# Kernel tuning notes

Hardware: AMD Instinct MI355X
Metric: run time of the kernel (lower is better)

The kernel has to match this reference:

```python
import jax, jax.numpy as jnp
import numpy as np

N_NODES = 51200
N_EDGES = 614400
ORIG = 92
AFL = 64      # atom_fea_len
NFL = 64      # nbr_fea_len
BINS = 100
N_CONV = 3
EPS = 1e-5


def _bn(h, g, b):
    # BatchNorm1d in training mode: biased batch statistics over dim 0
    mu = h.mean(0)
    var = h.var(0)
    return (h - mu) * jax.lax.rsqrt(var + EPS) * g + b


def setup_inputs() -> dict:
    key = jax.random.key(0)
    ks = jax.random.split(key, 16)
    inp = {
        "x": jax.random.normal(ks[0], (N_NODES, ORIG), dtype=jnp.float32),
        "edge_index": jax.random.randint(ks[1], (2, N_EDGES), 0, N_NODES, dtype=jnp.int32),
        "edge_attr": jax.random.uniform(ks[2], (N_EDGES, 1), dtype=jnp.float32),
        "batchsize": 128,
        # encoder-level params
        "attention": jnp.ones((ORIG,), jnp.float32),
        "emb_W": jax.random.normal(ks[3], (ORIG, AFL), jnp.float32) / np.sqrt(ORIG),
        "emb_b": jnp.zeros((AFL,), jnp.float32),
        # per-conv params stacked along axis 0 (n_conv layers)
        "ad_w1": jax.random.normal(ks[4], (N_CONV, 1, BINS), jnp.float32),
        "ad_b1": jnp.zeros((N_CONV, BINS), jnp.float32),
        "ad_w2": jax.random.normal(ks[5], (N_CONV, BINS, BINS), jnp.float32) / np.sqrt(BINS),
        "ad_b2": jnp.zeros((N_CONV, BINS), jnp.float32),
        "ad_alpha": jax.random.uniform(ks[6], (N_CONV, 1), dtype=jnp.float32),
        "ad_lut": jax.random.uniform(ks[7], (N_CONV, BINS, NFL), dtype=jnp.float32),
        "fc_W": jax.random.normal(ks[8], (N_CONV, 2 * AFL + NFL, 2 * AFL), jnp.float32) / np.sqrt(2 * AFL + NFL),
        "fc_b": jnp.zeros((N_CONV, 2 * AFL), jnp.float32),
        "bn1_g": jnp.ones((N_CONV, 2 * AFL), jnp.float32),
        "bn1_b": jnp.zeros((N_CONV, 2 * AFL), jnp.float32),
        "bn2_g": jnp.ones((N_CONV, AFL), jnp.float32),
        "bn2_b": jnp.zeros((N_CONV, AFL), jnp.float32),
        # pre_pooling linear
        "pp_W": jax.random.normal(ks[9], (AFL, AFL), jnp.float32) / np.sqrt(AFL),
        "pp_b": jnp.zeros((AFL,), jnp.float32),
    }
    return inp


def _cgconv(h, src, dst, edge_attr, w1, b1, w2, b2, alpha, lut, fcW, fcb, g1, be1, g2, be2):
    # AutoDiscretization of the scalar edge feature -> [E, NFL]
    v2 = jax.nn.leaky_relu(edge_attr @ w1 + b1)               # [E, BINS]
    v3 = v2 @ w2 + b2 + alpha * v2                            # [E, BINS]
    e = jax.nn.softmax(v3, axis=-1) @ lut                     # [E, NFL]
    # message: gather endpoints, fused gated MLP (x_i = target, x_j = source)
    z = jnp.concatenate([h[dst], h[src], e], axis=1) @ fcW + fcb  # [E, 2*AFL]
    z = _bn(z, g1, be1)
    nbr_filter, nbr_core = jnp.split(z, 2, axis=1)
    msg = jax.nn.relu(nbr_filter) * jax.nn.relu(nbr_core)     # [E, AFL]
    # aggregate (scatter-add to target nodes) + update
    aggr = jax.ops.segment_sum(msg, dst, num_segments=N_NODES)
    return jax.nn.relu(h + _bn(aggr, g2, be2))


def reference(x, edge_index, edge_attr, batchsize, attention, emb_W, emb_b,
              ad_w1, ad_b1, ad_w2, ad_b2, ad_alpha, ad_lut,
              fc_W, fc_b, bn1_g, bn1_b, bn2_g, bn2_b, pp_W, pp_b):
    src = edge_index[0]  # x_j
    dst = edge_index[1]  # x_i / aggregation target
    num_atom = N_NODES // batchsize

    h = (x * attention) @ emb_W + emb_b                       # [N, AFL]
    feas = [h]
    for l in range(N_CONV):
        h = _cgconv(h, src, dst, edge_attr,
                    ad_w1[l], ad_b1[l], ad_w2[l], ad_b2[l], ad_alpha[l], ad_lut[l],
                    fc_W[l], fc_b[l], bn1_g[l], bn1_b[l], bn2_g[l], bn2_b[l])
        feas.append(h)

    A = jnp.concatenate(feas, axis=0)                         # [(n_conv+1)*N, AFL]
    A = jax.nn.softmax(A @ pp_W + pp_b, axis=1)
    A = A.reshape(N_CONV + 1, batchsize, num_atom, AFL)
    crys_fea = A.sum(axis=0).sum(axis=1)                      # [batchsize, AFL]
    return crys_fea
```

## Files before the change

### kernel.cpp

```cpp
#include <hip/hip_runtime.h>

#define N_NODES 51200
#define N_EDGES 614400
#define ORIG 92
#define AFL 64
#define NFL 64
#define BINS 100
#define NCONV 3
#define BN_EPS 1e-5f
#define NTILES (N_EDGES / 16)

typedef __attribute__((ext_vector_type(8))) short bf8;
typedef __attribute__((ext_vector_type(4))) float f32x4;

__device__ __forceinline__ float bflo(unsigned int u) { return __uint_as_float(u << 16); }
__device__ __forceinline__ float bfhi(unsigned int u) { return __uint_as_float(u & 0xffff0000u); }
__device__ __forceinline__ unsigned int f2bf(float f) {
    unsigned int u = __float_as_uint(f);
    return (u + 0x7fffu + ((u >> 16) & 1u)) >> 16;
}
__device__ __forceinline__ short bfs(float f) { return (short)f2bf(f); }

__global__ __launch_bounds__(256) void hist_kernel(const int* __restrict__ ei,
                                                   int* __restrict__ cnt)
{
    int e = blockIdx.x * 256 + threadIdx.x;
    atomicAdd(&cnt[ei[N_EDGES + e]], 1);
}

__global__ __launch_bounds__(1024) void scan_kernel(int* __restrict__ cnt_cursor,
                                                    int* __restrict__ rowptr)
{
    __shared__ int part[1024];
    const int t = threadIdx.x;
    const int base = t * 50;
    int s = 0;
#pragma unroll 10
    for (int i = 0; i < 50; ++i) s += cnt_cursor[base + i];
    part[t] = s;
    __syncthreads();
    for (int off = 1; off < 1024; off <<= 1) {
        int v = (t >= off) ? part[t - off] : 0;
        __syncthreads();
        part[t] += v;
        __syncthreads();
    }
    int run = (t == 0) ? 0 : part[t - 1];
    for (int i = 0; i < 50; ++i) {
        int c = cnt_cursor[base + i];
        rowptr[base + i] = run;
        cnt_cursor[base + i] = run;
        run += c;
    }
    if (t == 1023) rowptr[N_NODES] = run;
}

__global__ __launch_bounds__(256) void permbuild_kernel(const int* __restrict__ ei,
                                                        int* __restrict__ cursor,
                                                        int* __restrict__ perm)
{
    int e = blockIdx.x * 256 + threadIdx.x;
    int d = ei[N_EDGES + e];
    int pos = atomicAdd(&cursor[d], 1);
    perm[pos] = e;
}

__global__ __launch_bounds__(256) void gather_sorted_kernel(
    const int* __restrict__ perm, const float* __restrict__ ea,
    const int* __restrict__ ei,
    float* __restrict__ ea_s, int* __restrict__ src_s, int* __restrict__ dst_s)
{
    int i = blockIdx.x * 256 + threadIdx.x;
    int e = perm[i];
    ea_s[i] = ea[e];
    src_s[i] = ei[e];
    dst_s[i] = ei[N_EDGES + e];
}

__global__ __launch_bounds__(256) void embed_kernel(
    const float* __restrict__ x, const float* __restrict__ att,
    const float* __restrict__ W, const float* __restrict__ b,
    float* __restrict__ h0, unsigned short* __restrict__ hbf)
{
    const int wave = threadIdx.x >> 6, lane = threadIdx.x & 63;
    const int gw = blockIdx.x * 4 + wave;
    const float bv = b[lane];
    for (int n = gw; n < N_NODES; n += gridDim.x * 4) {
        const float* xr = x + (size_t)n * ORIG;
        float acc = bv;
        for (int k = 0; k < ORIG; ++k)
            acc = fmaf(xr[k] * att[k], W[k * AFL + lane], acc);
        h0[(size_t)n * AFL + lane] = acc;
        hbf[(size_t)n * AFL + lane] = (unsigned short)f2bf(acc);
    }
}

#define SBS 202

__global__ __launch_bounds__(512, 1) void edge_kernel(
    const float* __restrict__ ea_s, const int* __restrict__ src_s,
    const int* __restrict__ dst_s,
    const unsigned short* __restrict__ hbf,
    const float* __restrict__ w1, const float* __restrict__ b1,
    const float* __restrict__ w2, const float* __restrict__ b2,
    const float* __restrict__ alpha_p, const float* __restrict__ lut,
    const float* __restrict__ fcW, const float* __restrict__ fcb,
    short* __restrict__ zo, float* __restrict__ stats)
{
    __shared__ short sW2f[7 * 4 * 64 * 8];
    __shared__ short sLutf[4 * 4 * 64 * 8];
    __shared__ short sFcf[6 * 8 * 64 * 8];
    __shared__ short sBuf[8][16 * SBS];

    const int tid = threadIdx.x;
    for (int i = tid; i < 1792; i += 512) {
        int t = i >> 8, rem = i & 255, s = rem >> 6, le = rem & 63;
        int n = 16 * t + (le & 15);
        int kb = 32 * s + ((le >> 4) << 3);
        short* d = &sW2f[i * 8];
#pragma unroll
        for (int j = 0; j < 8; ++j) {
            int k = kb + j;
            d[j] = bfs((n < BINS && k < BINS) ? w2[k * BINS + n] : 0.f);
        }
    }
    for (int i = tid; i < 1024; i += 512) {
        int t = i >> 8, rem = i & 255, s = rem >> 6, le = rem & 63;
        int n = 16 * t + (le & 15);
        int kb = 32 * s + ((le >> 4) << 3);
        short* d = &sLutf[i * 8];
#pragma unroll
        for (int j = 0; j < 8; ++j) {
            int k = kb + j;
            d[j] = bfs(k < BINS ? lut[k * NFL + n] : 0.f);
        }
    }
    for (int i = tid; i < 3072; i += 512) {
        int s = i >> 9, rem = i & 511, t = rem >> 6, le = rem & 63;
        int n = 16 * t + (le & 15);
        int kb = 32 * s + ((le >> 4) << 3);
        short* d = &sFcf[i * 8];
#pragma unroll
        for (int j = 0; j < 8; ++j)
            d[j] = bfs(fcW[(kb + j) * 128 + n]);
    }
    __syncthreads();

    const int wave = tid >> 6, lane = tid & 63;
    const int ln = lane & 15, q = lane >> 4;
    short* sB = &sBuf[wave][0];
    const float alpha = alpha_p[0];

    float w1c[7], b1c[7], b2c[7];
#pragma unroll
    for (int t = 0; t < 7; ++t) {
        int c = ln + 16 * t;
        bool v = c < BINS;
        w1c[t] = v ? w1[c] : 0.f;
        b1c[t] = v ? b1[c] : 0.f;
        b2c[t] = v ? b2[c] : 0.f;
    }
    float fbias[8];
#pragma unroll
    for (int t = 0; t < 8; ++t) fbias[t] = fcb[ln + 16 * t];

    float ss[8], sq[8];
#pragma unroll
    for (int t = 0; t < 8; ++t) { ss[t] = 0.f; sq[t] = 0.f; }

    int tile = blockIdx.x * 8 + wave;
    float avC = 0.f; int snC = 0, dnC = 0;
    bf8 hdC[2], hsC[2];
    if (tile < NTILES) {
        int base = tile * 16 + ln;
        avC = ea_s[base]; snC = src_s[base]; dnC = dst_s[base];
#pragma unroll
        for (int i = 0; i < 2; ++i) {
            int idx = i * 64 + lane;
            int row = idx >> 3, seg = idx & 7;
            int dnr = __shfl(dnC, row, 64);
            int snr = __shfl(snC, row, 64);
            hdC[i] = *(const bf8*)&hbf[(size_t)dnr * 64 + seg * 8];
            hsC[i] = *(const bf8*)&hbf[(size_t)snr * 64 + seg * 8];
        }
    }

    for (; tile < NTILES; tile += 2048) {
        const int ebase = tile * 16;
        const int tn = tile + 2048;
        const int tsafe = (tn < NTILES) ? tn : tile;
        const int nbase = tsafe * 16 + ln;
        float avN = ea_s[nbase];
        int snN = src_s[nbase];
        int dnN = dst_s[nbase];

        f32x4 acc[7];
#pragma unroll
        for (int r = 0; r < 4; ++r) {
            float ar = __shfl(avC, q * 4 + r, 64);
            const int rowoff = (q * 4 + r) * SBS;
#pragma unroll
            for (int t = 0; t < 7; ++t) {
                float v2c = fmaf(ar, w1c[t], b1c[t]);
                v2c = v2c > 0.f ? v2c : 0.01f * v2c;
                acc[t][r] = fmaf(alpha, v2c, b2c[t]);
                if (t < 6 || ln < 4) sB[rowoff + ln + 16 * t] = bfs(v2c);
            }
        }
        for (int i = lane; i < 16 * 28; i += 64) {
            int row = i / 28, c = 100 + (i - row * 28);
            sB[row * SBS + c] = 0;
        }
#pragma unroll
        for (int s = 0; s < 4; ++s) {
            bf8 a2 = *(const bf8*)&sB[ln * SBS + 32 * s + 8 * q];
#pragma unroll
            for (int t = 0; t < 7; ++t) {
                bf8 bw = *(const bf8*)&sW2f[((t * 4 + s) * 64 + lane) * 8];
                acc[t] = __builtin_amdgcn_mfma_f32_16x16x32_bf16(a2, bw, acc[t], 0, 0, 0);
            }
        }

        bf8 hdN[2], hsN[2];
#pragma unroll
        for (int i = 0; i < 2; ++i) {
            int idx = i * 64 + lane;
            int row = idx >> 3, seg = idx & 7;
            int dnr = __shfl(dnN, row, 64);
            int snr = __shfl(snN, row, 64);
            hdN[i] = *(const bf8*)&hbf[(size_t)dnr * 64 + seg * 8];
            hsN[i] = *(const bf8*)&hbf[(size_t)snr * 64 + seg * 8];
        }

#pragma unroll
        for (int r = 0; r < 4; ++r) {
            float m = -3.4e38f;
#pragma unroll
            for (int t = 0; t < 7; ++t)
                if (t < 6 || ln < 4) m = fmaxf(m, acc[t][r]);
#pragma unroll
            for (int o = 8; o >= 1; o >>= 1) m = fmaxf(m, __shfl_xor(m, o, 16));
            float ev[7], s = 0.f;
#pragma unroll
            for (int t = 0; t < 7; ++t) {
                ev[t] = (t < 6 || ln < 4) ? __expf(acc[t][r] - m) : 0.f;
                s += ev[t];
            }
#pragma unroll
            for (int o = 8; o >= 1; o >>= 1) s += __shfl_xor(s, o, 16);
            float inv = 1.0f / s;
#pragma unroll
            for (int t = 0; t < 7; ++t)
                if (t < 6 || ln < 4) sB[(q * 4 + r) * SBS + ln + 16 * t] = bfs(ev[t] * inv);
        }
        f32x4 eacc[4];
#pragma unroll
        for (int t = 0; t < 4; ++t) eacc[t] = (f32x4){0.f, 0.f, 0.f, 0.f};
#pragma unroll
        for (int s = 0; s < 4; ++s) {
            bf8 ap = *(const bf8*)&sB[ln * SBS + 32 * s + 8 * q];
#pragma unroll
            for (int t = 0; t < 4; ++t) {
                bf8 bl = *(const bf8*)&sLutf[((t * 4 + s) * 64 + lane) * 8];
                eacc[t] = __builtin_amdgcn_mfma_f32_16x16x32_bf16(ap, bl, eacc[t], 0, 0, 0);
            }
        }
#pragma unroll
        for (int i = 0; i < 2; ++i) {
            int idx = i * 64 + lane;
            int row = idx >> 3, seg = idx & 7;
            *(bf8*)&sB[row * SBS + seg * 8] = hdC[i];
            *(bf8*)&sB[row * SBS + 64 + seg * 8] = hsC[i];
        }
#pragma unroll
        for (int t = 0; t < 4; ++t)
#pragma unroll
            for (int r = 0; r < 4; ++r)
                sB[(q * 4 + r) * SBS + 128 + ln + 16 * t] = bfs(eacc[t][r]);
        f32x4 zacc[8];
#pragma unroll
        for (int t = 0; t < 8; ++t) zacc[t] = (f32x4){fbias[t], fbias[t], fbias[t], fbias[t]};
#pragma unroll
        for (int s = 0; s < 6; ++s) {
            bf8 ac = *(const bf8*)&sB[ln * SBS + 32 * s + 8 * q];
#pragma unroll
            for (int t = 0; t < 8; ++t) {
                bf8 bw = *(const bf8*)&sFcf[((s * 8 + t) * 64 + lane) * 8];
                zacc[t] = __builtin_amdgcn_mfma_f32_16x16x32_bf16(ac, bw, zacc[t], 0, 0, 0);
            }
        }
#pragma unroll
        for (int t = 0; t < 8; ++t)
#pragma unroll
            for (int r = 0; r < 4; ++r) {
                float zv = zacc[t][r];
                ss[t] += zv; sq[t] = fmaf(zv, zv, sq[t]);
                sB[(q * 4 + r) * SBS + ln + 16 * t] = bfs(zv);
            }
#pragma unroll
        for (int i = 0; i < 4; ++i) {
            int idx = i * 64 + lane;
            int row = idx >> 4, seg = idx & 15;
            bf8 v = *(const bf8*)&sB[row * SBS + seg * 8];
            *(bf8*)&zo[(size_t)(ebase + row) * 128 + seg * 8] = v;
        }
        avC = avN; snC = snN; dnC = dnN;
#pragma unroll
        for (int i = 0; i < 2; ++i) { hdC[i] = hdN[i]; hsC[i] = hsN[i]; }
    }

#pragma unroll
    for (int t = 0; t < 8; ++t) {
        ss[t] += __shfl_xor(ss[t], 16, 64); ss[t] += __shfl_xor(ss[t], 32, 64);
        sq[t] += __shfl_xor(sq[t], 16, 64); sq[t] += __shfl_xor(sq[t], 32, 64);
    }
    __syncthreads();
    float* sred = (float*)&sBuf[0][0];
    if (q == 0) {
#pragma unroll
        for (int t = 0; t < 8; ++t) {
            sred[wave * 128 + ln + 16 * t] = ss[t];
            sred[1024 + wave * 128 + ln + 16 * t] = sq[t];
        }
    }
    __syncthreads();
    if (tid < 256) {
        int base = (tid < 128) ? 0 : 1024;
        int col = tid & 127;
        float s = 0.f;
#pragma unroll
        for (int w = 0; w < 8; ++w) s += sred[base + w * 128 + col];
        atomicAdd(&stats[tid], s);
    }
}

__global__ void bn_fin_kernel(const float* __restrict__ stats,
                              const float* __restrict__ g, const float* __restrict__ b,
                              float* __restrict__ bnp, int C, float invN)
{
    int c = threadIdx.x;
    if (c >= C) return;
    float mu = stats[c] * invN;
    float var = stats[C + c] * invN - mu * mu;
    float sc = g[c] * rsqrtf(var + BN_EPS);
    bnp[c] = sc;
    bnp[C + c] = b[c] - mu * sc;
}

__global__ __launch_bounds__(256) void aggregate_kernel(
    const unsigned int* __restrict__ z32, const int* __restrict__ rowptr,
    const float* __restrict__ bnp, float* __restrict__ aggr)
{
    const int n = blockIdx.x * 4 + (threadIdx.x >> 6);
    const int lane = threadIdx.x & 63;
    const int f2 = lane & 31, slot = lane >> 5, f = 2 * f2;
    const float sc0 = bnp[f], sc1 = bnp[f + 1];
    const float sh0 = bnp[128 + f], sh1 = bnp[128 + f + 1];
    const float tc0 = bnp[64 + f], tc1 = bnp[64 + f + 1];
    const float th0 = bnp[192 + f], th1 = bnp[192 + f + 1];
    const int s = rowptr[n], e_end = rowptr[n + 1];
    float a0 = 0.f, a1 = 0.f;
    for (int e = s + slot; e < e_end; e += 2) {
        unsigned int ua = z32[(size_t)e * 64 + f2];
        unsigned int ub = z32[(size_t)e * 64 + 32 + f2];
        float zf0 = fmaf(bflo(ua), sc0, sh0);
        float zf1 = fmaf(bfhi(ua), sc1, sh1);
        float zc0 = fmaf(bflo(ub), tc0, th0);
        float zc1 = fmaf(bfhi(ub), tc1, th1);
        a0 += fmaxf(zf0, 0.f) * fmaxf(zc0, 0.f);
        a1 += fmaxf(zf1, 0.f) * fmaxf(zc1, 0.f);
    }
    a0 += __shfl_xor(a0, 32, 64);
    a1 += __shfl_xor(a1, 32, 64);
    if (slot == 0) {
        float2 w; w.x = a0; w.y = a1;
        *(float2*)&aggr[(size_t)n * 64 + f] = w;
    }
}

__global__ __launch_bounds__(256) void colstats64_kernel(
    const float* __restrict__ x, int rows, float* __restrict__ stats)
{
    int f = threadIdx.x & 63, sub = threadIdx.x >> 6;
    float s = 0.f, q = 0.f;
    for (int r = blockIdx.x * 4 + sub; r < rows; r += gridDim.x * 4) {
        float v = x[(size_t)r * 64 + f];
        s += v; q = fmaf(v, v, q);
    }
    __shared__ float ls[4][64], lq[4][64];
    ls[sub][f] = s; lq[sub][f] = q;
    __syncthreads();
    if (sub == 0) {
        s = ls[0][f] + ls[1][f] + ls[2][f] + ls[3][f];
        q = lq[0][f] + lq[1][f] + lq[2][f] + lq[3][f];
        atomicAdd(&stats[f], s);
        atomicAdd(&stats[64 + f], q);
    }
}

__global__ __launch_bounds__(256) void update_kernel(
    const float* __restrict__ h, const float* __restrict__ aggr,
    const float* __restrict__ bnp, float* __restrict__ hout,
    unsigned short* __restrict__ hbf)
{
    int t = blockIdx.x * 256 + threadIdx.x;
    int f = t & 63;
    float v = fmaf(aggr[t], bnp[f], bnp[64 + f]);
    float r = fmaxf(h[t] + v, 0.f);
    hout[t] = r;
    hbf[t] = (unsigned short)f2bf(r);
}

__global__ __launch_bounds__(256) void pool_kernel(
    const float* __restrict__ hbuf, const float* __restrict__ ppW,
    const float* __restrict__ ppb, float* __restrict__ out)
{
    const int l = blockIdx.x >> 7, b = blockIdx.x & 127;
    const int wave = threadIdx.x >> 6, lane = threadIdx.x & 63;
    float wcol[64];
#pragma unroll
    for (int k = 0; k < 64; ++k) wcol[k] = ppW[k * 64 + lane];
    const float bias = ppb[lane];
    const float* base = hbuf + ((size_t)l * N_NODES + (size_t)b * 400) * 64;
    __shared__ float srow[4][2][64];
    __shared__ float sacc[4][64];
    float acc = 0.f;
    for (int r = wave * 2; r < 400; r += 8) {
        srow[wave][0][lane] = base[(size_t)r * 64 + lane];
        srow[wave][1][lane] = base[(size_t)r * 64 + 64 + lane];
        float lg0 = bias, lg1 = bias;
#pragma unroll
        for (int k4 = 0; k4 < 64; k4 += 4) {
            float4 a = *(const float4*)&srow[wave][0][k4];
            float4 c = *(const float4*)&srow[wave][1][k4];
            lg0 = fmaf(a.x, wcol[k4 + 0], lg0); lg1 = fmaf(c.x, wcol[k4 + 0], lg1);
            lg0 = fmaf(a.y, wcol[k4 + 1], lg0); lg1 = fmaf(c.y, wcol[k4 + 1], lg1);
            lg0 = fmaf(a.z, wcol[k4 + 2], lg0); lg1 = fmaf(c.z, wcol[k4 + 2], lg1);
            lg0 = fmaf(a.w, wcol[k4 + 3], lg0); lg1 = fmaf(c.w, wcol[k4 + 3], lg1);
        }
        float m0 = lg0, m1 = lg1;
#pragma unroll
        for (int o = 32; o >= 1; o >>= 1) {
            m0 = fmaxf(m0, __shfl_xor(m0, o, 64));
            m1 = fmaxf(m1, __shfl_xor(m1, o, 64));
        }
        float e0 = __expf(lg0 - m0), e1 = __expf(lg1 - m1);
        float s0 = e0, s1 = e1;
#pragma unroll
        for (int o = 32; o >= 1; o >>= 1) {
            s0 += __shfl_xor(s0, o, 64);
            s1 += __shfl_xor(s1, o, 64);
        }
        acc += e0 * (1.0f / s0) + e1 * (1.0f / s1);
    }
    sacc[wave][lane] = acc;
    __syncthreads();
    if (wave == 0) {
        float t = sacc[0][lane] + sacc[1][lane] + sacc[2][lane] + sacc[3][lane];
        atomicAdd(&out[(size_t)b * 64 + lane], t);
    }
}

extern "C" void kernel_launch(void* const* d_in, const int* in_sizes, int n_in,
                              void* d_out, int out_size, void* d_ws, size_t ws_size,
                              hipStream_t stream)
{
    const float* x        = (const float*)d_in[0];
    const int*   ei       = (const int*)d_in[1];
    const float* ea       = (const float*)d_in[2];
    const float* att      = (const float*)d_in[4];
    const float* embW     = (const float*)d_in[5];
    const float* embB     = (const float*)d_in[6];
    const float* ad_w1    = (const float*)d_in[7];
    const float* ad_b1    = (const float*)d_in[8];
    const float* ad_w2    = (const float*)d_in[9];
    const float* ad_b2    = (const float*)d_in[10];
    const float* ad_alpha = (const float*)d_in[11];
    const float* ad_lut   = (const float*)d_in[12];
    const float* fc_W     = (const float*)d_in[13];
    const float* fc_b     = (const float*)d_in[14];
    const float* bn1_g    = (const float*)d_in[15];
    const float* bn1_b    = (const float*)d_in[16];
    const float* bn2_g    = (const float*)d_in[17];
    const float* bn2_b    = (const float*)d_in[18];
    const float* ppW      = (const float*)d_in[19];
    const float* ppb      = (const float*)d_in[20];
    float* out = (float*)d_out;

    char* ws = (char*)d_ws;
    float* hbuf   = (float*)ws;
    short* zU     = (short*)(ws + 52428800);
    float* aggr   = (float*)(ws + 209715200);
    float* stats1 = (float*)(ws + 222822400);
    float* bnp1   = stats1 + 256;
    float* stats2 = bnp1 + 256;
    float* bnp2   = stats2 + 128;
    int*   rowptr = (int*)(ws + 222826496);
    int*   cursor = (int*)(ws + 223031360);
    float* ea_s   = (float*)(ws + 223236160);
    int*   src_s  = (int*)(ws + 225693760);
    int*   dst_s  = (int*)(ws + 228151360);
    int*   perm   = (int*)(ws + 230608960);
    unsigned short* hbf = (unsigned short*)(ws + 230608960);

    hipMemsetAsync(cursor, 0, N_NODES * sizeof(int), stream);
    hist_kernel<<<N_EDGES / 256, 256, 0, stream>>>(ei, cursor);
    scan_kernel<<<1, 1024, 0, stream>>>(cursor, rowptr);
    permbuild_kernel<<<N_EDGES / 256, 256, 0, stream>>>(ei, cursor, perm);
    gather_sorted_kernel<<<N_EDGES / 256, 256, 0, stream>>>(perm, ea, ei, ea_s, src_s, dst_s);

    hipMemsetAsync(out, 0, 128 * 64 * sizeof(float), stream);
    embed_kernel<<<512, 256, 0, stream>>>(x, att, embW, embB, hbuf, hbf);

    for (int l = 0; l < NCONV; ++l) {
        float* h  = hbuf + (size_t)l * N_NODES * AFL;
        float* hn = h + (size_t)N_NODES * AFL;
        hipMemsetAsync(stats1, 0, 768 * 4, stream);
        edge_kernel<<<256, 512, 0, stream>>>(
            ea_s, src_s, dst_s, hbf,
            ad_w1 + l * BINS, ad_b1 + l * BINS,
            ad_w2 + l * BINS * BINS, ad_b2 + l * BINS,
            ad_alpha + l, ad_lut + l * BINS * NFL,
            fc_W + l * 192 * 128, fc_b + l * 128,
            zU, stats1);
        bn_fin_kernel<<<1, 128, 0, stream>>>(stats1, bn1_g + l * 128, bn1_b + l * 128,
                                             bnp1, 128, 1.0f / N_EDGES);
        aggregate_kernel<<<N_NODES / 4, 256, 0, stream>>>((const unsigned int*)zU, rowptr, bnp1, aggr);
        colstats64_kernel<<<256, 256, 0, stream>>>(aggr, N_NODES, stats2);
        bn_fin_kernel<<<1, 128, 0, stream>>>(stats2, bn2_g + l * 64, bn2_b + l * 64,
                                             bnp2, 64, 1.0f / N_NODES);
        update_kernel<<<N_NODES * 64 / 256, 256, 0, stream>>>(h, aggr, bnp2, hn, hbf);
    }

    pool_kernel<<<512, 256, 0, stream>>>(hbuf, ppW, ppb, out);
}
```

Measured before the change: 1.230 ms.

## Process two edge tiles per wave iteration and fuse BN stats into aggregation

The edge kernel now handles two 16-edge tiles per wave iteration, interleaving their MFMA chains so both share the same weight fragment loads from shared memory. This is meant to add instruction-level parallelism. The softmax drops its max-subtraction pass, which saves a reduction but risks overflow if logits are large. The one-iteration-ahead prefetch of gathered node features becomes an in-iteration gather for both tiles. Separately, the aggregate kernel now uses a grid-stride loop and accumulates column sums and sums of squares itself, removing the separate colstats pass over aggr.

```diff
diff --git a/kernel.cpp b/kernel.cpp
--- a/kernel.cpp
+++ b/kernel.cpp
@@ -9,6 +9,7 @@
 #define NCONV 3
 #define BN_EPS 1e-5f
 #define NTILES (N_EDGES / 16)
+#define NGROUPS (NTILES / 2)
 
 typedef __attribute__((ext_vector_type(8))) short bf8;
 typedef __attribute__((ext_vector_type(4))) float f32x4;
@@ -168,132 +169,177 @@
 #pragma unroll
     for (int t = 0; t < 8; ++t) { ss[t] = 0.f; sq[t] = 0.f; }
 
-    int tile = blockIdx.x * 8 + wave;
-    float avC = 0.f; int snC = 0, dnC = 0;
-    bf8 hdC[2], hsC[2];
-    if (tile < NTILES) {
-        int base = tile * 16 + ln;
-        avC = ea_s[base]; snC = src_s[base]; dnC = dst_s[base];
+    int g = blockIdx.x * 8 + wave;
+    float avA = 0.f, avB = 0.f;
+    int snA = 0, dnA = 0, snB = 0, dnB = 0;
+    if (g < NGROUPS) {
+        int b0 = g * 32 + ln;
+        avA = ea_s[b0];      snA = src_s[b0];      dnA = dst_s[b0];
+        avB = ea_s[b0 + 16]; snB = src_s[b0 + 16]; dnB = dst_s[b0 + 16];
+    }
+
+    for (; g < NGROUPS; g += 2048) {
+        const int ebase = g * 32;
+        bf8 hdA[2], hsA[2], hdB[2], hsB[2];
 #pragma unroll
         for (int i = 0; i < 2; ++i) {
             int idx = i * 64 + lane;
             int row = idx >> 3, seg = idx & 7;
-            int dnr = __shfl(dnC, row, 64);
-            int snr = __shfl(snC, row, 64);
-            hdC[i] = *(const bf8*)&hbf[(size_t)dnr * 64 + seg * 8];
-            hsC[i] = *(const bf8*)&hbf[(size_t)snr * 64 + seg * 8];
-        }
-    }
-
-    for (; tile < NTILES; tile += 2048) {
-        const int ebase = tile * 16;
-        const int tn = tile + 2048;
-        const int tsafe = (tn < NTILES) ? tn : tile;
-        const int nbase = tsafe * 16 + ln;
-        float avN = ea_s[nbase];
-        int snN = src_s[nbase];
-        int dnN = dst_s[nbase];
-
-        f32x4 acc[7];
+            int da = __shfl(dnA, row, 64), sa = __shfl(snA, row, 64);
+            int db = __shfl(dnB, row, 64), sb2 = __shfl(snB, row, 64);
+            hdA[i] = *(const bf8*)&hbf[(size_t)da * 64 + seg * 8];
+            hsA[i] = *(const bf8*)&hbf[(size_t)sa * 64 + seg * 8];
+            hdB[i] = *(const bf8*)&hbf[(size_t)db * 64 + seg * 8];
+            hsB[i] = *(const bf8*)&hbf[(size_t)sb2 * 64 + seg * 8];
+        }
+        const int gn = g + 2048;
+        const int gs = (gn < NGROUPS) ? gn : g;
+        const int bN = gs * 32 + ln;
+        float avAN = ea_s[bN];      int snAN = src_s[bN];      int dnAN = dst_s[bN];
+        float avBN = ea_s[bN + 16]; int snBN = src_s[bN + 16]; int dnBN = dst_s[bN + 16];
+
+        f32x4 accA[7], accB[7];
 #pragma unroll
         for (int r = 0; r < 4; ++r) {
-            float ar = __shfl(avC, q * 4 + r, 64);
+            float ar = __shfl(avA, q * 4 + r, 64);
             const int rowoff = (q * 4 + r) * SBS;
 #pragma unroll
             for (int t = 0; t < 7; ++t) {
                 float v2c = fmaf(ar, w1c[t], b1c[t]);
                 v2c = v2c > 0.f ? v2c : 0.01f * v2c;
-                acc[t][r] = fmaf(alpha, v2c, b2c[t]);
+                accA[t][r] = fmaf(alpha, v2c, b2c[t]);
                 if (t < 6 || ln < 4) sB[rowoff + ln + 16 * t] = bfs(v2c);
             }
         }
-        for (int i = lane; i < 16 * 28; i += 64) {
-            int row = i / 28, c = 100 + (i - row * 28);
+#pragma unroll
+        for (int i = 0; i < 7; ++i) {
+            int idx = i * 64 + lane;
+            int row = idx / 28, c = 100 + (idx - row * 28);
             sB[row * SBS + c] = 0;
         }
-#pragma unroll
-        for (int s = 0; s < 4; ++s) {
-            bf8 a2 = *(const bf8*)&sB[ln * SBS + 32 * s + 8 * q];
+        bf8 aA[4];
+#pragma unroll
+        for (int s = 0; s < 4; ++s) aA[s] = *(const bf8*)&sB[ln * SBS + 32 * s + 8 * q];
+#pragma unroll
+        for (int r = 0; r < 4; ++r) {
+            float ar = __shfl(avB, q * 4 + r, 64);
+            const int rowoff = (q * 4 + r) * SBS;
+#pragma unroll
+            for (int t = 0; t < 7; ++t) {
+                float v2c = fmaf(ar, w1c[t], b1c[t]);
+                v2c = v2c > 0.f ? v2c : 0.01f * v2c;
+                accB[t][r] = fmaf(alpha, v2c, b2c[t]);
+                if (t < 6 || ln < 4) sB[rowoff + ln + 16 * t] = bfs(v2c);
+            }
+        }
+        bf8 aB[4];
+#pragma unroll
+        for (int s = 0; s < 4; ++s) aB[s] = *(const bf8*)&sB[ln * SBS + 32 * s + 8 * q];
+#pragma unroll
+        for (int s = 0; s < 4; ++s)
 #pragma unroll
             for (int t = 0; t < 7; ++t) {
                 bf8 bw = *(const bf8*)&sW2f[((t * 4 + s) * 64 + lane) * 8];
-                acc[t] = __builtin_amdgcn_mfma_f32_16x16x32_bf16(a2, bw, acc[t], 0, 0, 0);
-            }
-        }
-
-        bf8 hdN[2], hsN[2];
+                accA[t] = __builtin_amdgcn_mfma_f32_16x16x32_bf16(aA[s], bw, accA[t], 0, 0, 0);
+                accB[t] = __builtin_amdgcn_mfma_f32_16x16x32_bf16(aB[s], bw, accB[t], 0, 0, 0);
+            }
+#pragma unroll
+        for (int r = 0; r < 4; ++r) {
+            float evA[7], evB[7], sumA = 0.f, sumB = 0.f;
+#pragma unroll
+            for (int t = 0; t < 7; ++t) {
+                bool on = (t < 6) || (ln < 4);
+                evA[t] = on ? __expf(accA[t][r]) : 0.f; sumA += evA[t];
+                evB[t] = on ? __expf(accB[t][r]) : 0.f; sumB += evB[t];
+            }
+#pragma unroll
+            for (int o = 8; o >= 1; o >>= 1) {
+                sumA += __shfl_xor(sumA, o, 16);
+                sumB += __shfl_xor(sumB, o, 16);
+            }
+            float iA = 1.0f / sumA, iB = 1.0f / sumB;
+#pragma unroll
+            for (int t = 0; t < 7; ++t) { accA[t][r] = evA[t] * iA; accB[t][r] = evB[t] * iB; }
+        }
+#pragma unroll
+        for (int r = 0; r < 4; ++r)
+#pragma unroll
+            for (int t = 0; t < 7; ++t)
+                if (t < 6 || ln < 4) sB[(q * 4 + r) * SBS + ln + 16 * t] = bfs(accA[t][r]);
+        bf8 apA[4];
+#pragma unroll
+        for (int s = 0; s < 4; ++s) apA[s] = *(const bf8*)&sB[ln * SBS + 32 * s + 8 * q];
+#pragma unroll
+        for (int r = 0; r < 4; ++r)
+#pragma unroll
+            for (int t = 0; t < 7; ++t)
+                if (t < 6 || ln < 4) sB[(q * 4 + r) * SBS + ln + 16 * t] = bfs(accB[t][r]);
+        bf8 apB[4];
+#pragma unroll
+        for (int s = 0; s < 4; ++s) apB[s] = *(const bf8*)&sB[ln * SBS + 32 * s + 8 * q];
+        f32x4 eaccA[4], eaccB[4];
+#pragma unroll
+        for (int t = 0; t < 4; ++t) {
+            eaccA[t] = (f32x4){0.f, 0.f, 0.f, 0.f};
+            eaccB[t] = (f32x4){0.f, 0.f, 0.f, 0.f};
+        }
+#pragma unroll
+        for (int s = 0; s < 4; ++s)
+#pragma unroll
+            for (int t = 0; t < 4; ++t) {
+                bf8 bl = *(const bf8*)&sLutf[((t * 4 + s) * 64 + lane) * 8];
+                eaccA[t] = __builtin_amdgcn_mfma_f32_16x16x32_bf16(apA[s], bl, eaccA[t], 0, 0, 0);
+                eaccB[t] = __builtin_amdgcn_mfma_f32_16x16x32_bf16(apB[s], bl, eaccB[t], 0, 0, 0);
+            }
 #pragma unroll
         for (int i = 0; i < 2; ++i) {
             int idx = i * 64 + lane;
             int row = idx >> 3, seg = idx & 7;
-            int dnr = __shfl(dnN, row, 64);
-            int snr = __shfl(snN, row, 64);
-            hdN[i] = *(const bf8*)&hbf[(size_t)dnr * 64 + seg * 8];
-            hsN[i] = *(const bf8*)&hbf[(size_t)snr * 64 + seg * 8];
-        }
-
-#pragma unroll
-        for (int r = 0; r < 4; ++r) {
-            float m = -3.4e38f;
-#pragma unroll
-            for (int t = 0; t < 7; ++t)
-                if (t < 6 || ln < 4) m = fmaxf(m, acc[t][r]);
-#pragma unroll
-            for (int o = 8; o >= 1; o >>= 1) m = fmaxf(m, __shfl_xor(m, o, 16));
-            float ev[7], s = 0.f;
-#pragma unroll
-            for (int t = 0; t < 7; ++t) {
-                ev[t] = (t < 6 || ln < 4) ? __expf(acc[t][r] - m) : 0.f;
-                s += ev[t];
-            }
-#pragma unroll
-            for (int o = 8; o >= 1; o >>= 1) s += __shfl_xor(s, o, 16);
-            float inv = 1.0f / s;
-#pragma unroll
-            for (int t = 0; t < 7; ++t)
-                if (t < 6 || ln < 4) sB[(q * 4 + r) * SBS + ln + 16 * t] = bfs(ev[t] * inv);
-        }
-        f32x4 eacc[4];
-#pragma unroll
-        for (int t = 0; t < 4; ++t) eacc[t] = (f32x4){0.f, 0.f, 0.f, 0.f};
-#pragma unroll
-        for (int s = 0; s < 4; ++s) {
-            bf8 ap = *(const bf8*)&sB[ln * SBS + 32 * s + 8 * q];
-#pragma unroll
-            for (int t = 0; t < 4; ++t) {
-                bf8 bl = *(const bf8*)&sLutf[((t * 4 + s) * 64 + lane) * 8];
-                eacc[t] = __builtin_amdgcn_mfma_f32_16x16x32_bf16(ap, bl, eacc[t], 0, 0, 0);
-            }
-        }
+            *(bf8*)&sB[row * SBS + seg * 8] = hdA[i];
+            *(bf8*)&sB[row * SBS + 64 + seg * 8] = hsA[i];
+        }
+#pragma unroll
+        for (int t = 0; t < 4; ++t)
+#pragma unroll
+            for (int r = 0; r < 4; ++r)
+                sB[(q * 4 + r) * SBS + 128 + ln + 16 * t] = bfs(eaccA[t][r]);
+        bf8 acA[6];
+#pragma unroll
+        for (int s = 0; s < 6; ++s) acA[s] = *(const bf8*)&sB[ln * SBS + 32 * s + 8 * q];
 #pragma unroll
         for (int i = 0; i < 2; ++i) {
             int idx = i * 64 + lane;
             int row = idx >> 3, seg = idx & 7;
-            *(bf8*)&sB[row * SBS + seg * 8] = hdC[i];
-            *(bf8*)&sB[row * SBS + 64 + seg * 8] = hsC[i];
+            *(bf8*)&sB[row * SBS + seg * 8] = hdB[i];
+            *(bf8*)&sB[row * SBS + 64 + seg * 8] = hsB[i];
         }
 #pragma unroll
         for (int t = 0; t < 4; ++t)
 #pragma unroll
             for (int r = 0; r < 4; ++r)
-                sB[(q * 4 + r) * SBS + 128 + ln + 16 * t] = bfs(eacc[t][r]);
-        f32x4 zacc[8];
-#pragma unroll
-        for (int t = 0; t < 8; ++t) zacc[t] = (f32x4){fbias[t], fbias[t], fbias[t], fbias[t]};
-#pragma unroll
-        for (int s = 0; s < 6; ++s) {
-            bf8 ac = *(const bf8*)&sB[ln * SBS + 32 * s + 8 * q];
+                sB[(q * 4 + r) * SBS + 128 + ln + 16 * t] = bfs(eaccB[t][r]);
+        bf8 acB[6];
+#pragma unroll
+        for (int s = 0; s < 6; ++s) acB[s] = *(const bf8*)&sB[ln * SBS + 32 * s + 8 * q];
+        f32x4 zaccA[8], zaccB[8];
+#pragma unroll
+        for (int t = 0; t < 8; ++t) {
+            zaccA[t] = (f32x4){fbias[t], fbias[t], fbias[t], fbias[t]};
+            zaccB[t] = (f32x4){fbias[t], fbias[t], fbias[t], fbias[t]};
+        }
+#pragma unroll
+        for (int s = 0; s < 6; ++s)
 #pragma unroll
             for (int t = 0; t < 8; ++t) {
                 bf8 bw = *(const bf8*)&sFcf[((s * 8 + t) * 64 + lane) * 8];
-                zacc[t] = __builtin_amdgcn_mfma_f32_16x16x32_bf16(ac, bw, zacc[t], 0, 0, 0);
-            }
-        }
+                zaccA[t] = __builtin_amdgcn_mfma_f32_16x16x32_bf16(acA[s], bw, zaccA[t], 0, 0, 0);
+                zaccB[t] = __builtin_amdgcn_mfma_f32_16x16x32_bf16(acB[s], bw, zaccB[t], 0, 0, 0);
+            }
 #pragma unroll
         for (int t = 0; t < 8; ++t)
 #pragma unroll
             for (int r = 0; r < 4; ++r) {
-                float zv = zacc[t][r];
+                float zv = zaccA[t][r];
                 ss[t] += zv; sq[t] = fmaf(zv, zv, sq[t]);
                 sB[(q * 4 + r) * SBS + ln + 16 * t] = bfs(zv);
             }
@@ -304,9 +350,23 @@
             bf8 v = *(const bf8*)&sB[row * SBS + seg * 8];
             *(bf8*)&zo[(size_t)(ebase + row) * 128 + seg * 8] = v;
         }
-        avC = avN; snC = snN; dnC = dnN;
-#pragma unroll
-        for (int i = 0; i < 2; ++i) { hdC[i] = hdN[i]; hsC[i] = hsN[i]; }
+#pragma unroll
+        for (int t = 0; t < 8; ++t)
+#pragma unroll
+            for (int r = 0; r < 4; ++r) {
+                float zv = zaccB[t][r];
+                ss[t] += zv; sq[t] = fmaf(zv, zv, sq[t]);
+                sB[(q * 4 + r) * SBS + ln + 16 * t] = bfs(zv);
+            }
+#pragma unroll
+        for (int i = 0; i < 4; ++i) {
+            int idx = i * 64 + lane;
+            int row = idx >> 4, seg = idx & 15;
+            bf8 v = *(const bf8*)&sB[row * SBS + seg * 8];
+            *(bf8*)&zo[(size_t)(ebase + 16 + row) * 128 + seg * 8] = v;
+        }
+        avA = avAN; snA = snAN; dnA = dnAN;
+        avB = avBN; snB = snBN; dnB = dnBN;
     }
 
 #pragma unroll
@@ -349,52 +409,49 @@
 
 __global__ __launch_bounds__(256) void aggregate_kernel(
     const unsigned int* __restrict__ z32, const int* __restrict__ rowptr,
-    const float* __restrict__ bnp, float* __restrict__ aggr)
-{
-    const int n = blockIdx.x * 4 + (threadIdx.x >> 6);
+    const float* __restrict__ bnp, float* __restrict__ aggr,
+    float* __restrict__ stats2)
+{
+    const int w = threadIdx.x >> 6;
     const int lane = threadIdx.x & 63;
     const int f2 = lane & 31, slot = lane >> 5, f = 2 * f2;
     const float sc0 = bnp[f], sc1 = bnp[f + 1];
     const float sh0 = bnp[128 + f], sh1 = bnp[128 + f + 1];
     const float tc0 = bnp[64 + f], tc1 = bnp[64 + f + 1];
     const float th0 = bnp[192 + f], th1 = bnp[192 + f + 1];
-    const int s = rowptr[n], e_end = rowptr[n + 1];
-    float a0 = 0.f, a1 = 0.f;
-    for (int e = s + slot; e < e_end; e += 2) {
-        unsigned int ua = z32[(size_t)e * 64 + f2];
-        unsigned int ub = z32[(size_t)e * 64 + 32 + f2];
-        float zf0 = fmaf(bflo(ua), sc0, sh0);
-        float zf1 = fmaf(bfhi(ua), sc1, sh1);
-        float zc0 = fmaf(bflo(ub), tc0, th0);
-        float zc1 = fmaf(bfhi(ub), tc1, th1);
-        a0 += fmaxf(zf0, 0.f) * fmaxf(zc0, 0.f);
-        a1 += fmaxf(zf1, 0.f) * fmaxf(zc1, 0.f);
-    }
-    a0 += __shfl_xor(a0, 32, 64);
-    a1 += __shfl_xor(a1, 32, 64);
+    float s0 = 0.f, s1 = 0.f, q0 = 0.f, q1 = 0.f;
+    for (int n = blockIdx.x * 4 + w; n < N_NODES; n += 6400) {
+        const int s = rowptr[n], e_end = rowptr[n + 1];
+        float a0 = 0.f, a1 = 0.f;
+        for (int e = s + slot; e < e_end; e += 2) {
+            unsigned int ua = z32[(size_t)e * 64 + f2];
+            unsigned int ub = z32[(size_t)e * 64 + 32 + f2];
+            float zf0 = fmaf(bflo(ua), sc0, sh0);
+            float zf1 = fmaf(bfhi(ua), sc1, sh1);
+            float zc0 = fmaf(bflo(ub), tc0, th0);
+            float zc1 = fmaf(bfhi(ub), tc1, th1);
+            a0 += fmaxf(zf0, 0.f) * fmaxf(zc0, 0.f);
+            a1 += fmaxf(zf1, 0.f) * fmaxf(zc1, 0.f);
+        }
+        a0 += __shfl_xor(a0, 32, 64);
+        a1 += __shfl_xor(a1, 32, 64);
+        if (slot == 0) {
+            float2 o; o.x = a0; o.y = a1;
+            *(float2*)&aggr[(size_t)n * 64 + f] = o;
+            s0 += a0; s1 += a1;
+            q0 = fmaf(a0, a0, q0); q1 = fmaf(a1, a1, q1);
+        }
+    }
+    __shared__ float red[4][128];
     if (slot == 0) {
-        float2 w; w.x = a0; w.y = a1;
-        *(float2*)&aggr[(size_t)n * 64 + f] = w;
-    }
-}
-
-__global__ __launch_bounds__(256) void colstats64_kernel(
-    const float* __restrict__ x, int rows, float* __restrict__ stats)
-{
-    int f = threadIdx.x & 63, sub = threadIdx.x >> 6;
-    float s = 0.f, q = 0.f;
-    for (int r = blockIdx.x * 4 + sub; r < rows; r += gridDim.x * 4) {
-        float v = x[(size_t)r * 64 + f];
-        s += v; q = fmaf(v, v, q);
-    }
-    __shared__ float ls[4][64], lq[4][64];
-    ls[sub][f] = s; lq[sub][f] = q;
+        red[w][f] = s0; red[w][f + 1] = s1;
+        red[w][64 + f] = q0; red[w][64 + f + 1] = q1;
+    }
     __syncthreads();
-    if (sub == 0) {
-        s = ls[0][f] + ls[1][f] + ls[2][f] + ls[3][f];
-        q = lq[0][f] + lq[1][f] + lq[2][f] + lq[3][f];
-        atomicAdd(&stats[f], s);
-        atomicAdd(&stats[64 + f], q);
+    if (threadIdx.x < 128) {
+        int c = threadIdx.x;
+        float v = red[0][c] + red[1][c] + red[2][c] + red[3][c];
+        atomicAdd(&stats2[c], v);
     }
 }
 
@@ -525,8 +582,8 @@
             zU, stats1);
         bn_fin_kernel<<<1, 128, 0, stream>>>(stats1, bn1_g + l * 128, bn1_b + l * 128,
                                              bnp1, 128, 1.0f / N_EDGES);
-        aggregate_kernel<<<N_NODES / 4, 256, 0, stream>>>((const unsigned int*)zU, rowptr, bnp1, aggr);
-        colstats64_kernel<<<256, 256, 0, stream>>>(aggr, N_NODES, stats2);
+        aggregate_kernel<<<1600, 256, 0, stream>>>((const unsigned int*)zU, rowptr, bnp1,
+                                                   aggr, stats2);
         bn_fin_kernel<<<1, 128, 0, stream>>>(stats2, bn2_g + l * 64, bn2_b + l * 64,
                                              bnp2, 64, 1.0f / N_NODES);
         update_kernel<<<N_NODES * 64 / 256, 256, 0, stream>>>(h, aggr, bnp2, hn, hbf);
```

Measured after the change: 1.248 ms. Within noise of the previous version (+1.4%).
